# Performance work log

Measured on AMD Instinct MI355X. Metric: run time of the kernel, lower is better.

## Reference

```python
import jax, jax.numpy as jnp
import numpy as np

MARGIN = 0.2
MAX_VIOLATION = False
REDUCTION = 'mean'

N, D = 8192, 512


def setup_inputs() -> dict:
    key = jax.random.key(0)
    k1, k2, k3 = jax.random.split(key, 3)
    im = jax.random.normal(k1, (N, D), dtype=jnp.float32)
    s = jax.random.normal(k2, (N, D), dtype=jnp.float32)
    ex_s = jax.random.normal(k3, (N, D), dtype=jnp.float32)
    return {"im": im, "s": s, "ex_s": ex_s}


def l2_sim(im, s):
    # scores[i, j] = -||im_i - s_j||_2, computed via the GEMM identity
    # ||a-b||^2 = ||a||^2 + ||b||^2 - 2 a.b (same math, no NxNxD intermediate)
    im_sq = jnp.sum(im * im, axis=1)            # [N_im]
    s_sq = jnp.sum(s * s, axis=1)               # [N_s]
    d2 = im_sq[:, None] + s_sq[None, :] - 2.0 * (im @ s.T)  # [N_im, N_s]
    return -jnp.sqrt(jnp.maximum(d2, 0.0))


def reference(im, s, ex_s):
    scores = l2_sim(im, ex_s)        # [N_im, N_ex]
    scores_orig = l2_sim(im, s)      # [N_im, N_im]
    diagonal = jnp.diagonal(scores_orig)[:, None]            # [N_im, 1]
    cost_s = jnp.maximum(MARGIN + scores - diagonal, 0.0)    # [N_im, N_ex]
    if MAX_VIOLATION:
        cost_s = jnp.max(cost_s, axis=1)
    if REDUCTION == 'mean':
        return jnp.mean(cost_s)
    return jnp.sum(cost_s)
```

## Files before the change

### kernel.cpp

```cpp
#include <hip/hip_runtime.h>
#include <hip/hip_bf16.h>

#define NROW 8192
#define DDIM 512
#define MARGIN 0.2f

typedef __bf16 bf16x8 __attribute__((ext_vector_type(8)));
typedef float f32x4 __attribute__((ext_vector_type(4)));

__device__ __forceinline__ void gload16(const void* g, void* l) {
    __builtin_amdgcn_global_load_lds(
        (const __attribute__((address_space(1))) void*)g,
        (__attribute__((address_space(3))) void*)l, 16, 0, 0);
}

#define BAR() __builtin_amdgcn_s_barrier()
#define LGKM0() asm volatile("s_waitcnt lgkmcnt(0)" ::: "memory")

__global__ __launch_bounds__(256) void prep_kernel(
    const float* __restrict__ im, const float* __restrict__ s,
    const float* __restrict__ ex,
    ushort* __restrict__ Abf, ushort* __restrict__ Bbf,
    float2* __restrict__ idat, float* __restrict__ exsq) {
    int b = blockIdx.x;
    bool isim = b < NROW;
    int row = isim ? b : b - NROW;
    const float* src = isim ? im : ex;
    ushort* dst = isim ? Abf : Bbf;
    int tid = threadIdx.x;

    float2 v = ((const float2*)(src + (size_t)row * DDIM))[tid];
    __hip_bfloat16 hx = __float2bfloat16(v.x);
    __hip_bfloat16 hy = __float2bfloat16(v.y);
    unsigned packed = (unsigned)*(const ushort*)&hx | ((unsigned)*(const ushort*)&hy << 16);
    ((unsigned*)(dst + (size_t)row * DDIM))[tid] = packed;

    float ssq = v.x * v.x + v.y * v.y;
    float dsq = 0.f;
    if (isim) {
        float2 sv = ((const float2*)(s + (size_t)row * DDIM))[tid];
        float dx = v.x - sv.x, dy = v.y - sv.y;
        dsq = dx * dx + dy * dy;
    }
    #pragma unroll
    for (int off = 32; off > 0; off >>= 1) {
        ssq += __shfl_down(ssq, off);
        dsq += __shfl_down(dsq, off);
    }
    __shared__ float sred[8];
    int lane = tid & 63, w = tid >> 6;
    if (lane == 0) { sred[w] = ssq; sred[4 + w] = dsq; }
    __syncthreads();
    if (tid == 0) {
        float S = sred[0] + sred[1] + sred[2] + sred[3];
        float Dd = sred[4] + sred[5] + sred[6] + sred[7];
        if (isim) idat[row] = make_float2(S, MARGIN + sqrtf(Dd));
        else      exsq[row] = S;
    }
}

__global__ __launch_bounds__(512) void gemm_cost_kernel(
    const ushort* __restrict__ Abf, const ushort* __restrict__ Bbf,
    const float2* __restrict__ idat, const float* __restrict__ exsq,
    float* __restrict__ partials) {
    __shared__ __align__(16) ushort sA[2][16384];
    __shared__ __align__(16) ushort sB[2][16384];
    __shared__ float redbuf[8];

    int bid0 = blockIdx.x;
    int c = bid0 & 7;
    int sq = bid0 >> 3;
    int bi = c * 4 + (sq & 3);
    int bj = (sq >> 5) * 8 + ((sq >> 2) & 7);
    int bid = bi * 32 + bj;
    int ibase = bi * 256, jbase = bj * 256;
    int tid = threadIdx.x, lane = tid & 63, w = tid >> 6;
    int wr = w >> 2, wc = w & 3;

    int r = tid >> 3;
    int pc = tid & 7;
    int lc = pc ^ (r & 7);
    const ushort* aG = Abf + (size_t)(ibase + r) * DDIM + lc * 8;
    const ushort* bG = Bbf + (size_t)(jbase + r) * DDIM + lc * 8;
    ushort* aL = &sA[0][0] + r * 64 + pc * 8;
    ushort* bL = &sB[0][0] + r * 64 + pc * 8;

    auto STAGE = [&](int h) {
        if (h >= 32) return;
        int kt = h >> 2, q = h & 3;
        if (q < 2) {
            const ushort* g = aG + q * (128 * DDIM) + kt * 64;
            ushort* l = aL + (kt & 1) * 16384 + q * 8192;
            gload16(g, l);
            gload16(g + 64 * DDIM, l + 4096);
        } else {
            int qq = q - 2;
            const ushort* g = bG + qq * (128 * DDIM) + kt * 64;
            ushort* l = bL + (kt & 1) * 16384 + qq * 8192;
            gload16(g, l);
            gload16(g + 64 * DDIM, l + 4096);
        }
    };

    int l15 = lane & 15;
    int pc0 = (((lane >> 4) ^ (lane & 7)) * 8);
    int pc1 = pc0 ^ 32;
    int aoff = (wr * 128 + l15) * 64;
    int boff = (wc * 64 + l15) * 64;

    f32x4 acc[8][4] = {};

    STAGE(0); STAGE(1); STAGE(2); STAGE(3);
    STAGE(4); STAGE(5); STAGE(6); STAGE(7);
    asm volatile("s_waitcnt vmcnt(8)" ::: "memory");
    BAR();

    #pragma unroll
    for (int t = 0; t < 8; ++t) {
        const ushort* pA = &sA[t & 1][0];
        const ushort* pB = &sB[t & 1][0];
        bf16x8 a0[4][2], a1[4][2], b0[2][2], b1[2][2];

        #pragma unroll
        for (int m = 0; m < 4; ++m) {
            a0[m][0] = *(const bf16x8*)(pA + aoff + m * 1024 + pc0);
            a0[m][1] = *(const bf16x8*)(pA + aoff + m * 1024 + pc1);
        }
        #pragma unroll
        for (int n = 0; n < 2; ++n) {
            b0[n][0] = *(const bf16x8*)(pB + boff + n * 1024 + pc0);
            b0[n][1] = *(const bf16x8*)(pB + boff + n * 1024 + pc1);
        }
        BAR(); LGKM0();
        __builtin_amdgcn_s_setprio(1);
        #pragma unroll
        for (int m = 0; m < 4; ++m)
            #pragma unroll
            for (int n = 0; n < 2; ++n) {
                acc[m][n] = __builtin_amdgcn_mfma_f32_16x16x32_bf16(a0[m][0], b0[n][0], acc[m][n], 0, 0, 0);
                acc[m][n] = __builtin_amdgcn_mfma_f32_16x16x32_bf16(a0[m][1], b0[n][1], acc[m][n], 0, 0, 0);
            }
        __builtin_amdgcn_s_setprio(0);
        BAR();

        #pragma unroll
        for (int m = 0; m < 4; ++m) {
            a1[m][0] = *(const bf16x8*)(pA + aoff + (m + 4) * 1024 + pc0);
            a1[m][1] = *(const bf16x8*)(pA + aoff + (m + 4) * 1024 + pc1);
        }
        BAR(); LGKM0();
        __builtin_amdgcn_s_setprio(1);
        #pragma unroll
        for (int m = 0; m < 4; ++m)
            #pragma unroll
            for (int n = 0; n < 2; ++n) {
                acc[m + 4][n] = __builtin_amdgcn_mfma_f32_16x16x32_bf16(a1[m][0], b0[n][0], acc[m + 4][n], 0, 0, 0);
                acc[m + 4][n] = __builtin_amdgcn_mfma_f32_16x16x32_bf16(a1[m][1], b0[n][1], acc[m + 4][n], 0, 0, 0);
            }
        __builtin_amdgcn_s_setprio(0);
        BAR();

        #pragma unroll
        for (int n = 0; n < 2; ++n) {
            b1[n][0] = *(const bf16x8*)(pB + boff + (n + 2) * 1024 + pc0);
            b1[n][1] = *(const bf16x8*)(pB + boff + (n + 2) * 1024 + pc1);
        }
        STAGE(4 * (t + 2) + 0);
        STAGE(4 * (t + 2) + 1);
        BAR(); LGKM0();
        __builtin_amdgcn_s_setprio(1);
        #pragma unroll
        for (int m = 0; m < 4; ++m)
            #pragma unroll
            for (int n = 0; n < 2; ++n) {
                acc[m][n + 2] = __builtin_amdgcn_mfma_f32_16x16x32_bf16(a0[m][0], b1[n][0], acc[m][n + 2], 0, 0, 0);
                acc[m][n + 2] = __builtin_amdgcn_mfma_f32_16x16x32_bf16(a0[m][1], b1[n][1], acc[m][n + 2], 0, 0, 0);
            }
        __builtin_amdgcn_s_setprio(0);
        BAR();

        STAGE(4 * (t + 2) + 2);
        STAGE(4 * (t + 2) + 3);
        BAR();
        __builtin_amdgcn_s_setprio(1);
        #pragma unroll
        for (int m = 0; m < 4; ++m)
            #pragma unroll
            for (int n = 0; n < 2; ++n) {
                acc[m + 4][n + 2] = __builtin_amdgcn_mfma_f32_16x16x32_bf16(a1[m][0], b1[n][0], acc[m + 4][n + 2], 0, 0, 0);
                acc[m + 4][n + 2] = __builtin_amdgcn_mfma_f32_16x16x32_bf16(a1[m][1], b1[n][1], acc[m + 4][n + 2], 0, 0, 0);
            }
        __builtin_amdgcn_s_setprio(0);
        if (t < 6)       asm volatile("s_waitcnt vmcnt(8)" ::: "memory");
        else if (t == 6) asm volatile("s_waitcnt vmcnt(0)" ::: "memory");
        BAR();
    }

    float jt[4];
    #pragma unroll
    for (int n = 0; n < 4; ++n) jt[n] = exsq[jbase + wc * 64 + n * 16 + l15];
    int r0 = (lane >> 4) * 4;
    float lsum = 0.f;
    #pragma unroll
    for (int m = 0; m < 8; ++m) {
        #pragma unroll
        for (int rg = 0; rg < 4; ++rg) {
            int i = ibase + wr * 128 + m * 16 + r0 + rg;
            float2 id = idat[i];
            #pragma unroll
            for (int n = 0; n < 4; ++n) {
                float d2 = fmaxf(id.x + jt[n] - 2.0f * acc[m][n][rg], 0.0f);
                lsum += fmaxf(id.y - sqrtf(d2), 0.0f);
            }
        }
    }
    #pragma unroll
    for (int off = 32; off > 0; off >>= 1) lsum += __shfl_down(lsum, off);
    if (lane == 0) redbuf[w] = lsum;
    __syncthreads();
    if (tid == 0) {
        float tot = 0.f;
        #pragma unroll
        for (int q = 0; q < 8; ++q) tot += redbuf[q];
        partials[bid] = tot;
    }
}

__global__ __launch_bounds__(256) void finalize_kernel(
    const float* __restrict__ partials, float* __restrict__ out) {
    float acc = 0.f;
    for (int t = threadIdx.x; t < 1024; t += 256) acc += partials[t];
    #pragma unroll
    for (int off = 32; off > 0; off >>= 1) acc += __shfl_down(acc, off);
    __shared__ float sred[4];
    int lane = threadIdx.x & 63, w = threadIdx.x >> 6;
    if (lane == 0) sred[w] = acc;
    __syncthreads();
    if (threadIdx.x == 0) {
        float total = sred[0] + sred[1] + sred[2] + sred[3];
        out[0] = total * (1.0f / (8192.0f * 8192.0f));
    }
}

extern "C" void kernel_launch(void* const* d_in, const int* in_sizes, int n_in,
                              void* d_out, int out_size, void* d_ws, size_t ws_size,
                              hipStream_t stream) {
    const float* im = (const float*)d_in[0];
    const float* s  = (const float*)d_in[1];
    const float* ex = (const float*)d_in[2];

    char* ws = (char*)d_ws;
    ushort* Abf   = (ushort*)(ws);
    ushort* Bbf   = (ushort*)(ws + 8388608);
    float2* idat  = (float2*)(ws + 16777216);
    float*  exsq  = (float*)(ws + 16842752);
    float*  parts = (float*)(ws + 16875520);

    prep_kernel<<<2 * NROW, 256, 0, stream>>>(im, s, ex, Abf, Bbf, idat, exsq);
    gemm_cost_kernel<<<(NROW / 256) * (NROW / 256), 512, 0, stream>>>(Abf, Bbf, idat, exsq, parts);
    finalize_kernel<<<1, 256, 0, stream>>>(parts, (float*)d_out);
}
```

Before: 109.2 us.

## Collapse four-phase ping-pong main loop into two MFMA phases with batched staging

```diff
diff --git a/kernel.cpp b/kernel.cpp
--- a/kernel.cpp
+++ b/kernel.cpp
@@ -15,7 +15,6 @@
 }
 
 #define BAR() __builtin_amdgcn_s_barrier()
-#define LGKM0() asm volatile("s_waitcnt lgkmcnt(0)" ::: "memory")
 
 __global__ __launch_bounds__(256) void prep_kernel(
     const float* __restrict__ im, const float* __restrict__ s,
@@ -119,78 +118,45 @@
     for (int t = 0; t < 8; ++t) {
         const ushort* pA = &sA[t & 1][0];
         const ushort* pB = &sB[t & 1][0];
-        bf16x8 a0[4][2], a1[4][2], b0[2][2], b1[2][2];
-
-        #pragma unroll
-        for (int m = 0; m < 4; ++m) {
-            a0[m][0] = *(const bf16x8*)(pA + aoff + m * 1024 + pc0);
-            a0[m][1] = *(const bf16x8*)(pA + aoff + m * 1024 + pc1);
+        bf16x8 a[8][2], b0[2][2], b1[2][2];
+
+        #pragma unroll
+        for (int m = 0; m < 8; ++m) {
+            a[m][0] = *(const bf16x8*)(pA + aoff + m * 1024 + pc0);
+            a[m][1] = *(const bf16x8*)(pA + aoff + m * 1024 + pc1);
         }
         #pragma unroll
         for (int n = 0; n < 2; ++n) {
             b0[n][0] = *(const bf16x8*)(pB + boff + n * 1024 + pc0);
             b0[n][1] = *(const bf16x8*)(pB + boff + n * 1024 + pc1);
         }
-        BAR(); LGKM0();
         __builtin_amdgcn_s_setprio(1);
         #pragma unroll
-        for (int m = 0; m < 4; ++m)
+        for (int m = 0; m < 8; ++m)
             #pragma unroll
             for (int n = 0; n < 2; ++n) {
-                acc[m][n] = __builtin_amdgcn_mfma_f32_16x16x32_bf16(a0[m][0], b0[n][0], acc[m][n], 0, 0, 0);
-                acc[m][n] = __builtin_amdgcn_mfma_f32_16x16x32_bf16(a0[m][1], b0[n][1], acc[m][n], 0, 0, 0);
+                acc[m][n] = __builtin_amdgcn_mfma_f32_16x16x32_bf16(a[m][0], b0[n][0], acc[m][n], 0, 0, 0);
+                acc[m][n] = __builtin_amdgcn_mfma_f32_16x16x32_bf16(a[m][1], b0[n][1], acc[m][n], 0, 0, 0);
             }
         __builtin_amdgcn_s_setprio(0);
-        BAR();
-
-        #pragma unroll
-        for (int m = 0; m < 4; ++m) {
-            a1[m][0] = *(const bf16x8*)(pA + aoff + (m + 4) * 1024 + pc0);
-            a1[m][1] = *(const bf16x8*)(pA + aoff + (m + 4) * 1024 + pc1);
-        }
-        BAR(); LGKM0();
-        __builtin_amdgcn_s_setprio(1);
-        #pragma unroll
-        for (int m = 0; m < 4; ++m)
-            #pragma unroll
-            for (int n = 0; n < 2; ++n) {
-                acc[m + 4][n] = __builtin_amdgcn_mfma_f32_16x16x32_bf16(a1[m][0], b0[n][0], acc[m + 4][n], 0, 0, 0);
-                acc[m + 4][n] = __builtin_amdgcn_mfma_f32_16x16x32_bf16(a1[m][1], b0[n][1], acc[m + 4][n], 0, 0, 0);
-            }
-        __builtin_amdgcn_s_setprio(0);
-        BAR();
-
         #pragma unroll
         for (int n = 0; n < 2; ++n) {
             b1[n][0] = *(const bf16x8*)(pB + boff + (n + 2) * 1024 + pc0);
             b1[n][1] = *(const bf16x8*)(pB + boff + (n + 2) * 1024 + pc1);
         }
-        STAGE(4 * (t + 2) + 0);
-        STAGE(4 * (t + 2) + 1);
-        BAR(); LGKM0();
         __builtin_amdgcn_s_setprio(1);
         #pragma unroll
-        for (int m = 0; m < 4; ++m)
+        for (int m = 0; m < 8; ++m)
             #pragma unroll
             for (int n = 0; n < 2; ++n) {
-                acc[m][n + 2] = __builtin_amdgcn_mfma_f32_16x16x32_bf16(a0[m][0], b1[n][0], acc[m][n + 2], 0, 0, 0);
-                acc[m][n + 2] = __builtin_amdgcn_mfma_f32_16x16x32_bf16(a0[m][1], b1[n][1], acc[m][n + 2], 0, 0, 0);
+                acc[m][n + 2] = __builtin_amdgcn_mfma_f32_16x16x32_bf16(a[m][0], b1[n][0], acc[m][n + 2], 0, 0, 0);
+                acc[m][n + 2] = __builtin_amdgcn_mfma_f32_16x16x32_bf16(a[m][1], b1[n][1], acc[m][n + 2], 0, 0, 0);
             }
         __builtin_amdgcn_s_setprio(0);
+
         BAR();
-
-        STAGE(4 * (t + 2) + 2);
-        STAGE(4 * (t + 2) + 3);
-        BAR();
-        __builtin_amdgcn_s_setprio(1);
-        #pragma unroll
-        for (int m = 0; m < 4; ++m)
-            #pragma unroll
-            for (int n = 0; n < 2; ++n) {
-                acc[m + 4][n + 2] = __builtin_amdgcn_mfma_f32_16x16x32_bf16(a1[m][0], b1[n][0], acc[m + 4][n + 2], 0, 0, 0);
-                acc[m + 4][n + 2] = __builtin_amdgcn_mfma_f32_16x16x32_bf16(a1[m][1], b1[n][1], acc[m + 4][n + 2], 0, 0, 0);
-            }
-        __builtin_amdgcn_s_setprio(0);
+        STAGE(4 * (t + 2) + 0); STAGE(4 * (t + 2) + 1);
+        STAGE(4 * (t + 2) + 2); STAGE(4 * (t + 2) + 3);
         if (t < 6)       asm volatile("s_waitcnt vmcnt(8)" ::: "memory");
         else if (t == 6) asm volatile("s_waitcnt vmcnt(0)" ::: "memory");
         BAR();
```

After: 109.4 us. No clear change (+0.2%).
